# Kernel optimization log

Measured on AMD Instinct MI355X. Metric: run time of the kernel, lower is better.

## Reference

```python
import jax, jax.numpy as jnp
import numpy as np

B, S, H, NH = 2, 2048, 1024, 16
HD = H // NH
EPS = 1e-6

def rotate_half(x):
    x1, x2 = jnp.split(x, 2, axis=-1)
    return jnp.concatenate([-x2, x1], axis=-1)

def setup_inputs() -> dict:
    key = jax.random.key(0)
    ks = jax.random.split(key, 4)
    x = jax.random.normal(ks[0], (B, S, H), dtype=jnp.float32)
    # rotary angles
    inv_freq = 1.0 / (10000.0 ** (np.arange(0, HD, 2, dtype=np.float32) / HD))
    t = np.arange(S, dtype=np.float32)
    freqs = np.einsum('s,d->sd', t, inv_freq)
    emb = np.concatenate([freqs, freqs], axis=-1)  # [S, HD]
    cos = jnp.broadcast_to(jnp.cos(emb)[None], (B, S, HD)).astype(jnp.float32)
    sin = jnp.broadcast_to(jnp.sin(emb)[None], (B, S, HD)).astype(jnp.float32)
    attn_mask = jnp.broadcast_to(jnp.tril(jnp.ones((S, S), jnp.float32))[None], (B, S, S))
    W_uvqk = jax.random.normal(ks[1], (4 * H, H), dtype=jnp.float32) * (1.0 / np.sqrt(H))
    b_uvqk = jnp.zeros((4 * H,), jnp.float32)
    gate_w = jnp.ones((H,), jnp.float32)
    W_out = jax.random.normal(ks[2], (H, H), dtype=jnp.float32) * (1.0 / np.sqrt(H))
    b_out = jnp.zeros((H,), jnp.float32)
    return {"x": x, "cos": cos, "sin": sin, "attn_mask": attn_mask,
            "W_uvqk": W_uvqk, "b_uvqk": b_uvqk, "gate_w": gate_w,
            "W_out": W_out, "b_out": b_out}

def reference(x, cos, sin, attn_mask, W_uvqk, b_uvqk, gate_w, W_out, b_out):
    b, s, h = x.shape
    residual = x
    uvqk = jnp.einsum('bsh,oh->bso', x, W_uvqk) + b_uvqk
    u, v, q, k = jnp.split(uvqk, 4, axis=-1)
    u = jax.nn.silu(u)
    q = q.reshape(b, s, NH, HD)
    k = k.reshape(b, s, NH, HD)
    v = v.reshape(b, s, NH, HD)
    c = cos[:, :, None, :]  # [B,S,1,HD] broadcasts over heads
    sn = sin[:, :, None, :]
    q = q * c + rotate_half(q) * sn
    k = k * c + rotate_half(k) * sn
    # [B,NH,S,S] raw scores -> silu (no softmax) -> mask -> AV
    scores = jnp.einsum('bqnd,bknd->bnqk', q, k) / np.sqrt(HD).astype(np.float32)
    attn = jax.nn.silu(scores) * attn_mask[:, None, :, :]
    attn_out = jnp.einsum('bnqk,bknd->bqnd', attn, v).reshape(b, s, h)
    # RMSNorm (fp32) gating
    ao32 = attn_out.astype(jnp.float32)
    var = jnp.mean(ao32 * ao32, axis=-1, keepdims=True)
    normed = (gate_w * (ao32 * jax.lax.rsqrt(var + EPS))).astype(x.dtype)
    gated = normed * u
    out = jnp.einsum('bsh,oh->bso', gated, W_out) + b_out
    return residual + out
```

## Files before the change

kernel.cpp:

```cpp
#include <hip/hip_runtime.h>

typedef __attribute__((ext_vector_type(4))) float f32x4;
typedef __attribute__((ext_vector_type(8))) short short8;

static __device__ __forceinline__ unsigned short f2bf(float f) {
    union { float f; unsigned int u; } v; v.f = f;
    unsigned int r = v.u + 0x7FFFu + ((v.u >> 16) & 1u);
    return (unsigned short)(r >> 16);
}

static __device__ __forceinline__ float bf2f(unsigned short h) {
    union { unsigned int u; float f; } v; v.u = ((unsigned int)h) << 16;
    return v.f;
}

static __device__ __forceinline__ unsigned int cvt_pk_bf16(float lo, float hi) {
    unsigned int r;
    asm("v_cvt_pk_bf16_f32 %0, %1, %2" : "=v"(r) : "v"(lo), "v"(hi));
    return r;
}

static __device__ __forceinline__ void gload16(const void* g, void* l) {
    __builtin_amdgcn_global_load_lds(
        (const __attribute__((address_space(1))) unsigned int*)g,
        (__attribute__((address_space(3))) unsigned int*)l, 16, 0, 0);
}

static __device__ __forceinline__ void block_sync_raw() {
    asm volatile("" ::: "memory");
    __builtin_amdgcn_s_barrier();
    asm volatile("" ::: "memory");
}

__global__ __launch_bounds__(256) void k_convert(
    const float* __restrict__ x, const float* __restrict__ wu, const float* __restrict__ wo,
    unsigned short* __restrict__ xb, unsigned short* __restrict__ wub, unsigned short* __restrict__ wob)
{
    int i = blockIdx.x * 256 + threadIdx.x;
    const float* src; unsigned short* dst; int off;
    if (i < 1048576)       { src = x;  dst = xb;  off = i; }
    else if (i < 2097152)  { src = wu; dst = wub; off = i - 1048576; }
    else                   { src = wo; dst = wob; off = i - 2097152; }
    float4 v = reinterpret_cast<const float4*>(src)[off];
    ushort4 o;
    o.x = f2bf(v.x); o.y = f2bf(v.y); o.z = f2bf(v.z); o.w = f2bf(v.w);
    reinterpret_cast<ushort4*>(dst)[off] = o;
}

__global__ __launch_bounds__(256) void k_gemm0(
    const unsigned short* __restrict__ A, const unsigned short* __restrict__ Bmat,
    const float* __restrict__ bias,
    unsigned short* __restrict__ u_out, unsigned short* __restrict__ q_out,
    unsigned short* __restrict__ k_out, unsigned short* __restrict__ vt_out,
    const float* __restrict__ cosp, const float* __restrict__ sinp)
{
    const int K = 1024;
    constexpr int NT = 16;
    constexpr int ASZ = 64 * 64;
    constexpr int BSZ = 128 * 64;
    __shared__ __align__(16) unsigned short S[2 * (ASZ + BSZ)];
    int tid = threadIdx.x;
    int lane = tid & 63, wid = tid >> 6;
    int lo = lane & 15, q4 = lane >> 4;
    int x7 = lo & 7;
    int wr = wid >> 1, wc = wid & 1;
    int bm = blockIdx.x, bn = blockIdx.y;
    const unsigned short* Abase = A + (size_t)bm * 64 * K;
    const unsigned short* Bbase = Bmat + (size_t)bn * 128 * K;

    auto stage = [&](int bb, int kt) {
        unsigned short* As = S + bb * (ASZ + BSZ);
        unsigned short* Bs = As + ASZ;
#pragma unroll
        for (int j = 0; j < 2; ++j) {
            int ch = tid + j * 256;
            int r = ch >> 3, p = ch & 7;
            gload16(Abase + (size_t)r * K + kt * 64 + (p ^ (r & 7)) * 8, As + ch * 8);
        }
#pragma unroll
        for (int j = 0; j < 4; ++j) {
            int ch = tid + j * 256;
            int r = ch >> 3, p = ch & 7;
            gload16(Bbase + (size_t)r * K + kt * 64 + (p ^ (r & 7)) * 8, Bs + ch * 8);
        }
    };

    f32x4 acc[2][4] = {};
    stage(0, 0);
    int buf = 0;
    for (int kt = 0; kt < NT; ++kt) {
        if (kt + 1 < NT) {
            stage(buf ^ 1, kt + 1);
            asm volatile("s_waitcnt vmcnt(6)" ::: "memory");
        } else {
            asm volatile("s_waitcnt vmcnt(0)" ::: "memory");
        }
        block_sync_raw();
        const unsigned short* As = S + buf * (ASZ + BSZ);
        const unsigned short* Bs = As + ASZ;
#pragma unroll
        for (int kc = 0; kc < 2; ++kc) {
            int cRd = (kc * 4 + q4) ^ x7;
            short8 af[2], bfr[4];
#pragma unroll
            for (int t = 0; t < 2; ++t)
                af[t] = *(const short8*)&As[(wr * 32 + t * 16 + lo) * 64 + cRd * 8];
#pragma unroll
            for (int t = 0; t < 4; ++t)
                bfr[t] = *(const short8*)&Bs[(wc * 64 + t * 16 + lo) * 64 + cRd * 8];
#pragma unroll
            for (int mt = 0; mt < 2; ++mt)
#pragma unroll
                for (int nt = 0; nt < 4; ++nt)
                    acc[mt][nt] = __builtin_amdgcn_mfma_f32_16x16x32_bf16(af[mt], bfr[nt], acc[mt][nt], 0, 0, 0);
        }
        block_sync_raw();
        buf ^= 1;
    }

    int rowb = bm * 64 + wr * 32;
    int colb = bn * 128 + wc * 64;
    int region = bn >> 3;
    if (region == 1) {
        unsigned short* T = S;
#pragma unroll
        for (int mt = 0; mt < 2; ++mt)
#pragma unroll
            for (int nt = 0; nt < 4; ++nt) {
                float bcol = bias[colb + nt * 16 + lo];
                uint2 w;
                w.x = cvt_pk_bf16(acc[mt][nt][0] + bcol, acc[mt][nt][1] + bcol);
                w.y = cvt_pk_bf16(acc[mt][nt][2] + bcol, acc[mt][nt][3] + bcol);
                int c_local = wc * 64 + nt * 16 + lo;
                int schunk = wr * 4 + mt * 2 + (q4 >> 1);
                *(uint2*)((char*)T + c_local * 128 + ((schunk ^ (c_local & 7)) * 16) + (q4 & 1) * 8) = w;
            }
        __syncthreads();
        int c_row = tid >> 1;
        int bchunk = (tid & 1) * 4;
        int c_global = (bn - 8) * 128 + c_row;
        int head = c_global >> 6, d = c_global & 63;
        int batch = bm >> 5;
        int s_base = (bm * 64) & 2047;
        unsigned short* vrow = vt_out + ((size_t)(batch * 16 + head) * 64 + d) * 2048;
#pragma unroll
        for (int i = 0; i < 4; ++i) {
            int chunk = bchunk + i;
            uint4 v = *(const uint4*)((const char*)T + c_row * 128 + ((chunk ^ (c_row & 7)) * 16));
            *(uint4*)&vrow[s_base + chunk * 8] = v;
        }
    } else {
#pragma unroll
        for (int mt = 0; mt < 2; ++mt) {
#pragma unroll
            for (int r = 0; r < 4; ++r) {
                int rg = rowb + mt * 16 + q4 * 4 + r;
                int b = rg >> 11, s = rg & 2047;
                float vals[4];
#pragma unroll
                for (int nt = 0; nt < 4; ++nt)
                    vals[nt] = acc[mt][nt][r] + bias[colb + nt * 16 + lo];
                if (region == 0) {
#pragma unroll
                    for (int nt = 0; nt < 4; ++nt) {
                        float vv = vals[nt];
                        u_out[(size_t)rg * 1024 + colb + nt * 16 + lo] = f2bf(vv / (1.f + __expf(-vv)));
                    }
                } else {
                    const float* cb = cosp + (size_t)(b * 2048 + s) * 64;
                    const float* sb = sinp + (size_t)(b * 2048 + s) * 64;
                    float o[4];
#pragma unroll
                    for (int nt = 0; nt < 4; ++nt) {
                        int hd = nt * 16 + lo;
                        float partner = (nt < 2) ? -vals[nt + 2] : vals[nt - 2];
                        o[nt] = vals[nt] * cb[hd] + partner * sb[hd];
                    }
                    int c0 = colb - ((region == 2) ? 2048 : 3072);
                    unsigned short* dst = (region == 2) ? q_out : k_out;
#pragma unroll
                    for (int nt = 0; nt < 4; ++nt) {
                        int c = c0 + nt * 16 + lo;
                        int head = c >> 6, d = c & 63;
                        dst[((size_t)(b * 16 + head) * 2048 + s) * 64 + d] = f2bf(o[nt]);
                    }
                }
            }
        }
    }
}

__global__ __launch_bounds__(256) void k_gemm1(
    const unsigned short* __restrict__ A, const unsigned short* __restrict__ Bmat,
    const float* __restrict__ bias, const float* __restrict__ resid, float* __restrict__ out)
{
    const int K = 1024;
    constexpr int NT = 16;
    constexpr int ASZ = 64 * 64;
    constexpr int BSZ = 128 * 64;
    __shared__ __align__(16) unsigned short S[2 * (ASZ + BSZ)];
    int tid = threadIdx.x;
    int lane = tid & 63, wid = tid >> 6;
    int lo = lane & 15, q4 = lane >> 4;
    int x7 = lo & 7;
    int wr = wid >> 1, wc = wid & 1;
    int bn = blockIdx.x, bm = blockIdx.y;
    const unsigned short* Abase = A + (size_t)bm * 64 * K;
    const unsigned short* Bbase = Bmat + (size_t)bn * 128 * K;

    auto stage = [&](int bb, int kt) {
        unsigned short* As = S + bb * (ASZ + BSZ);
        unsigned short* Bs = As + ASZ;
#pragma unroll
        for (int j = 0; j < 2; ++j) {
            int ch = tid + j * 256;
            int r = ch >> 3, p = ch & 7;
            gload16(Abase + (size_t)r * K + kt * 64 + (p ^ (r & 7)) * 8, As + ch * 8);
        }
#pragma unroll
        for (int j = 0; j < 4; ++j) {
            int ch = tid + j * 256;
            int r = ch >> 3, p = ch & 7;
            gload16(Bbase + (size_t)r * K + kt * 64 + (p ^ (r & 7)) * 8, Bs + ch * 8);
        }
    };

    f32x4 acc[2][4] = {};
    stage(0, 0);
    int buf = 0;
    for (int kt = 0; kt < NT; ++kt) {
        if (kt + 1 < NT) {
            stage(buf ^ 1, kt + 1);
            asm volatile("s_waitcnt vmcnt(6)" ::: "memory");
        } else {
            asm volatile("s_waitcnt vmcnt(0)" ::: "memory");
        }
        block_sync_raw();
        const unsigned short* As = S + buf * (ASZ + BSZ);
        const unsigned short* Bs = As + ASZ;
#pragma unroll
        for (int kc = 0; kc < 2; ++kc) {
            int cRd = (kc * 4 + q4) ^ x7;
            short8 af[2], bfr[4];
#pragma unroll
            for (int t = 0; t < 2; ++t)
                af[t] = *(const short8*)&As[(wr * 32 + t * 16 + lo) * 64 + cRd * 8];
#pragma unroll
            for (int t = 0; t < 4; ++t)
                bfr[t] = *(const short8*)&Bs[(wc * 64 + t * 16 + lo) * 64 + cRd * 8];
#pragma unroll
            for (int mt = 0; mt < 2; ++mt)
#pragma unroll
                for (int nt = 0; nt < 4; ++nt)
                    acc[mt][nt] = __builtin_amdgcn_mfma_f32_16x16x32_bf16(af[mt], bfr[nt], acc[mt][nt], 0, 0, 0);
        }
        block_sync_raw();
        buf ^= 1;
    }

    int rowb = bm * 64 + wr * 32;
    int colb = bn * 128 + wc * 64;
#pragma unroll
    for (int mt = 0; mt < 2; ++mt)
#pragma unroll
        for (int r = 0; r < 4; ++r) {
            int rg = rowb + mt * 16 + q4 * 4 + r;
#pragma unroll
            for (int nt = 0; nt < 4; ++nt) {
                int c = colb + nt * 16 + lo;
                out[(size_t)rg * 1024 + c] = acc[mt][nt][r] + bias[c] + resid[(size_t)rg * 1024 + c];
            }
        }
}

__global__ __launch_bounds__(256) void k_attn(
    const unsigned short* __restrict__ Q, const unsigned short* __restrict__ Kg,
    const unsigned short* __restrict__ Vt_g, unsigned short* __restrict__ AO0,
    unsigned short* __restrict__ AO1)
{
    __shared__ __align__(16) unsigned short Ksb[2][64 * 64];
    __shared__ __align__(16) unsigned short Vsb[2][64 * 64];
    __shared__ __align__(16) unsigned short Ps[4 * 2048];
    int tid = threadIdx.x;
    int lane = tid & 63, wid = tid >> 6;
    int lo = lane & 15, q4 = lane >> 4;
    int bid = blockIdx.x;
    int bh = bid & 31;
    int s  = bid >> 5;
    int b = bh >> 4, head = bh & 15;

    const unsigned short* Qb = Q    + (size_t)bh * 2048 * 64;
    const unsigned short* Kb = Kg   + (size_t)bh * 2048 * 64;
    const unsigned short* Vb = Vt_g + (size_t)bh * 64 * 2048;
    unsigned short* Pw = Ps + wid * 2048;

    int i0 = wid * 128 + lane;
    int i1 = wid * 128 + 64 + lane;
    int c_0 = i0 & 7, r_0 = i0 >> 3;
    int c_1 = i1 & 7, r_1 = i1 >> 3;
    int cs0 = c_0 ^ (r_0 & 7), cs1 = c_1 ^ (r_1 & 7);
    size_t kOff0 = (size_t)r_0 * 64 + cs0 * 8,  kOff1 = (size_t)r_1 * 64 + cs1 * 8;
    size_t vOff0 = (size_t)r_0 * 2048 + cs0 * 8, vOff1 = (size_t)r_1 * 2048 + cs1 * 8;

    int x7 = lo & 7, qr_rel = q4 >> 1;
    char* pw0 = (char*)Pw + (lo)      * 128 + (q4 & 1) * 8;
    char* pw1 = (char*)Pw + (lo + 16) * 128 + (q4 & 1) * 8;
    int swz[8];
#pragma unroll
    for (int cc = 0; cc < 8; ++cc) swz[cc] = (cc ^ x7) * 16;
    const short8* prd[2][2];
#pragma unroll
    for (int kc = 0; kc < 2; ++kc) {
        prd[0][kc] = (const short8*)&Pw[(lo) * 64      + (((kc * 4 + q4) ^ x7) * 8)];
        prd[1][kc] = (const short8*)&Pw[(16 + lo) * 64 + (((kc * 4 + q4) ^ x7) * 8)];
    }

    auto stage = [&](int bb, int kt) {
        gload16(Kb + (size_t)kt * 4096 + kOff0, &Ksb[bb][i0 * 8]);
        gload16(Kb + (size_t)kt * 4096 + kOff1, &Ksb[bb][i1 * 8]);
        gload16(Vb + (size_t)kt * 64 + vOff0, &Vsb[bb][i0 * 8]);
        gload16(Vb + (size_t)kt * 64 + vOff1, &Vsb[bb][i1 * 8]);
    };

    int J = s;
    int q0w = J * 128 + wid * 32;
    short8 qf[2][2];
#pragma unroll
    for (int qt = 0; qt < 2; ++qt)
#pragma unroll
        for (int kc = 0; kc < 2; ++kc)
            qf[qt][kc] = *(const short8*)(Qb + (size_t)(q0w + qt * 16 + lo) * 64 + kc * 32 + q4 * 8);

    f32x4 oacc[2][4] = {};
    stage(0, 0);
    __syncthreads();
    int buf = 0;

    for (int t = 0; t < 17; ++t) {
        int kt = (t <= s) ? t : (t + 15 - 2 * s);
        if (t < 16) {
            int tn = t + 1;
            int ktn = (tn <= s) ? tn : (tn + 15 - 2 * s);
            stage(buf ^ 1, ktn);
        }
        if (64 * kt <= q0w + 31) {
            f32x4 sacc[4][2] = {};
#pragma unroll
            for (int kc = 0; kc < 2; ++kc)
#pragma unroll
                for (int kt4 = 0; kt4 < 4; ++kt4) {
                    short8 kf = *(const short8*)&Ksb[buf][(kt4 * 16 + lo) * 64 + (((kc * 4 + q4) ^ x7) * 8)];
#pragma unroll
                    for (int qt = 0; qt < 2; ++qt)
                        sacc[kt4][qt] = __builtin_amdgcn_mfma_f32_16x16x32_bf16(kf, qf[qt][kc], sacc[kt4][qt], 0, 0, 0);
                }
            bool needMask = (64 * kt + 63 > q0w);
#pragma unroll
            for (int kt4 = 0; kt4 < 4; ++kt4)
#pragma unroll
                for (int qt = 0; qt < 2; ++qt) {
                    int qc = qt * 16 + lo;
                    float p[4];
#pragma unroll
                    for (int rr = 0; rr < 4; ++rr) {
                        float S = sacc[kt4][qt][rr];
                        float e = __builtin_amdgcn_exp2f(S * -0.180336880f);
                        float pv = S * 0.125f * __builtin_amdgcn_rcpf(1.f + e);
                        if (needMask) {
                            int ky = kt * 64 + kt4 * 16 + q4 * 4 + rr;
                            if (ky > q0w + qc) pv = 0.f;
                        }
                        p[rr] = pv;
                    }
                    uint2 w;
                    w.x = cvt_pk_bf16(p[0], p[1]);
                    w.y = cvt_pk_bf16(p[2], p[3]);
                    *(uint2*)(((qt == 0) ? pw0 : pw1) + swz[kt4 * 2 + qr_rel]) = w;
                }
#pragma unroll
            for (int kc = 0; kc < 2; ++kc) {
                short8 pf0 = *prd[0][kc];
                short8 pf1 = *prd[1][kc];
#pragma unroll
                for (int nt = 0; nt < 4; ++nt) {
                    short8 vf = *(const short8*)&Vsb[buf][(nt * 16 + lo) * 64 + (((kc * 4 + q4) ^ x7) * 8)];
                    oacc[0][nt] = __builtin_amdgcn_mfma_f32_16x16x32_bf16(pf0, vf, oacc[0][nt], 0, 0, 0);
                    oacc[1][nt] = __builtin_amdgcn_mfma_f32_16x16x32_bf16(pf1, vf, oacc[1][nt], 0, 0, 0);
                }
            }
        }
        if (t == s) {
            unsigned short* aoLane = AO0 + ((size_t)(b * 2048 + q0w + q4 * 4)) * 1024 + head * 64 + lo;
#pragma unroll
            for (int qt = 0; qt < 2; ++qt)
#pragma unroll
                for (int nt = 0; nt < 4; ++nt)
#pragma unroll
                    for (int rr = 0; rr < 4; ++rr) {
                        aoLane[(qt * 16 + rr) * 1024 + nt * 16] = f2bf(oacc[qt][nt][rr]);
                        oacc[qt][nt][rr] = 0.f;
                    }
            J = 15 - s;
            q0w = J * 128 + wid * 32;
#pragma unroll
            for (int qt = 0; qt < 2; ++qt)
#pragma unroll
                for (int kc = 0; kc < 2; ++kc)
                    qf[qt][kc] = *(const short8*)(Qb + (size_t)(q0w + qt * 16 + lo) * 64 + kc * 32 + q4 * 8);
        }
        __syncthreads();
        buf ^= 1;
    }
    unsigned short* aoLane = AO1 + ((size_t)(b * 2048 + q0w + q4 * 4)) * 1024 + head * 64 + lo;
#pragma unroll
    for (int qt = 0; qt < 2; ++qt)
#pragma unroll
        for (int nt = 0; nt < 4; ++nt)
#pragma unroll
            for (int rr = 0; rr < 4; ++rr)
                aoLane[(qt * 16 + rr) * 1024 + nt * 16] = f2bf(oacc[qt][nt][rr]);
}

__global__ __launch_bounds__(256) void k_rmsgate(
    const unsigned short* __restrict__ AO0, const unsigned short* __restrict__ AO1,
    const unsigned short* __restrict__ U,
    const float* __restrict__ gw, unsigned short* __restrict__ G)
{
    __shared__ float red[4];
    int row = blockIdx.x, t = threadIdx.x;
    ushort4 a0v = *(const ushort4*)&AO0[(size_t)row * 1024 + t * 4];
    ushort4 a1v = *(const ushort4*)&AO1[(size_t)row * 1024 + t * 4];
    float4 a;
    a.x = bf2f(a0v.x) + bf2f(a1v.x);
    a.y = bf2f(a0v.y) + bf2f(a1v.y);
    a.z = bf2f(a0v.z) + bf2f(a1v.z);
    a.w = bf2f(a0v.w) + bf2f(a1v.w);
    float ss = a.x * a.x + a.y * a.y + a.z * a.z + a.w * a.w;
#pragma unroll
    for (int off = 32; off; off >>= 1) ss += __shfl_down(ss, off);
    int wid = t >> 6, lane = t & 63;
    if (lane == 0) red[wid] = ss;
    __syncthreads();
    float tot = red[0] + red[1] + red[2] + red[3];
    float rs = rsqrtf(tot * (1.f / 1024.f) + 1e-6f);
    float4 g = *(const float4*)&gw[t * 4];
    ushort4 uv = *(const ushort4*)&U[(size_t)row * 1024 + t * 4];
    ushort4 o;
    o.x = f2bf(g.x * a.x * rs * bf2f(uv.x));
    o.y = f2bf(g.y * a.y * rs * bf2f(uv.y));
    o.z = f2bf(g.z * a.z * rs * bf2f(uv.z));
    o.w = f2bf(g.w * a.w * rs * bf2f(uv.w));
    *(ushort4*)&G[(size_t)row * 1024 + t * 4] = o;
}

extern "C" void kernel_launch(void* const* d_in, const int* in_sizes, int n_in,
                              void* d_out, int out_size, void* d_ws, size_t ws_size,
                              hipStream_t stream) {
    const float* x      = (const float*)d_in[0];
    const float* cosp   = (const float*)d_in[1];
    const float* sinp   = (const float*)d_in[2];
    const float* b_uvqk = (const float*)d_in[5];
    const float* gate_w = (const float*)d_in[6];
    const float* b_out  = (const float*)d_in[8];
    float* out = (float*)d_out;

    char* ws = (char*)d_ws;
    unsigned short* xb  = (unsigned short*)(ws);
    unsigned short* wub = (unsigned short*)(ws + 8388608);
    unsigned short* wob = (unsigned short*)(ws + 16777216);
    unsigned short* ub  = (unsigned short*)(ws + 18874368);
    unsigned short* qb  = (unsigned short*)(ws + 35651584);
    unsigned short* kb  = (unsigned short*)(ws + 44040192);
    unsigned short* vtb = (unsigned short*)(ws + 52428800);
    unsigned short* aob = (unsigned short*)(ws + 60817408);
    unsigned short* gb  = (unsigned short*)(ws + 77594624);
    unsigned short* ao1 = (unsigned short*)(ws);

    k_convert<<<9216, 256, 0, stream>>>((const float*)d_in[0], (const float*)d_in[4],
                                        (const float*)d_in[7], xb, wub, wob);
    k_gemm0<<<dim3(64, 32), 256, 0, stream>>>(xb, wub, b_uvqk, ub, qb, kb, vtb, cosp, sinp);
    k_attn<<<512, 256, 0, stream>>>(qb, kb, vtb, aob, ao1);
    k_rmsgate<<<4096, 256, 0, stream>>>(aob, ao1, ub, gate_w, gb);
    k_gemm1<<<dim3(8, 64), 256, 0, stream>>>(gb, wob, b_out, x, out);
}
```

Measured before the change: 120.9 us.

## Split attention KV loop across two blocks per tile with partial-sum buffers

Each attention block's 17-step key loop is split into two halves run by separate blocks (1024 blocks instead of 512). Each half writes its bf16 partial outputs, or zeros, into its own buffer pair, and the RMS-gate kernel sums four partials instead of two. This aims to fill more CUs on the MI355X and cut per-block latency. The cost is extra global writes and reads for the partials, extra rounding from storing partials in bf16, and reuse of the xb/wub workspace as scratch.

```diff
diff --git a/kernel.cpp b/kernel.cpp
--- a/kernel.cpp
+++ b/kernel.cpp
@@ -275,8 +275,9 @@
 
 __global__ __launch_bounds__(256) void k_attn(
     const unsigned short* __restrict__ Q, const unsigned short* __restrict__ Kg,
-    const unsigned short* __restrict__ Vt_g, unsigned short* __restrict__ AO0,
-    unsigned short* __restrict__ AO1)
+    const unsigned short* __restrict__ Vt_g,
+    unsigned short* __restrict__ P1a, unsigned short* __restrict__ P1b,
+    unsigned short* __restrict__ P2a, unsigned short* __restrict__ P2b)
 {
     __shared__ __align__(16) unsigned short Ksb[2][64 * 64];
     __shared__ __align__(16) unsigned short Vsb[2][64 * 64];
@@ -286,8 +287,12 @@
     int lo = lane & 15, q4 = lane >> 4;
     int bid = blockIdx.x;
     int bh = bid & 31;
-    int s  = bid >> 5;
+    int s  = (bid >> 5) & 15;
+    int h  = bid >> 9;
     int b = bh >> 4, head = bh & 15;
+    unsigned short* P1 = h ? P1b : P1a;
+    unsigned short* P2 = h ? P2b : P2a;
+    int t0 = h ? 9 : 0, t1 = h ? 17 : 9;
 
     const unsigned short* Qb = Q    + (size_t)bh * 2048 * 64;
     const unsigned short* Kb = Kg   + (size_t)bh * 2048 * 64;
@@ -321,8 +326,31 @@
         gload16(Vb + (size_t)kt * 64 + vOff0, &Vsb[bb][i0 * 8]);
         gload16(Vb + (size_t)kt * 64 + vOff1, &Vsb[bb][i1 * 8]);
     };
-
-    int J = s;
+    auto ktof = [&](int u) { return (u <= s) ? u : (u + 15 - 2 * s); };
+
+    f32x4 oacc[2][4] = {};
+    auto storeP = [&](unsigned short* bufp, int q0x) {
+        unsigned short* p = bufp + ((size_t)(b * 2048 + q0x + q4 * 4)) * 1024 + head * 64 + lo;
+#pragma unroll
+        for (int qt = 0; qt < 2; ++qt)
+#pragma unroll
+            for (int nt = 0; nt < 4; ++nt)
+#pragma unroll
+                for (int rr = 0; rr < 4; ++rr)
+                    p[(qt * 16 + rr) * 1024 + nt * 16] = f2bf(oacc[qt][nt][rr]);
+    };
+    auto zeroP = [&](unsigned short* bufp, int q0x) {
+        unsigned short* p = bufp + ((size_t)(b * 2048 + q0x + q4 * 4)) * 1024 + head * 64 + lo;
+#pragma unroll
+        for (int qt = 0; qt < 2; ++qt)
+#pragma unroll
+            for (int nt = 0; nt < 4; ++nt)
+#pragma unroll
+                for (int rr = 0; rr < 4; ++rr)
+                    p[(qt * 16 + rr) * 1024 + nt * 16] = 0;
+    };
+
+    int J = (t0 <= s) ? s : 15 - s;
     int q0w = J * 128 + wid * 32;
     short8 qf[2][2];
 #pragma unroll
@@ -331,18 +359,14 @@
         for (int kc = 0; kc < 2; ++kc)
             qf[qt][kc] = *(const short8*)(Qb + (size_t)(q0w + qt * 16 + lo) * 64 + kc * 32 + q4 * 8);
 
-    f32x4 oacc[2][4] = {};
-    stage(0, 0);
+    stage(0, ktof(t0));
     __syncthreads();
     int buf = 0;
-
-    for (int t = 0; t < 17; ++t) {
-        int kt = (t <= s) ? t : (t + 15 - 2 * s);
-        if (t < 16) {
-            int tn = t + 1;
-            int ktn = (tn <= s) ? tn : (tn + 15 - 2 * s);
-            stage(buf ^ 1, ktn);
-        }
+    bool stored1 = false;
+
+    for (int t = t0; t < t1; ++t) {
+        if (t + 1 < t1) stage(buf ^ 1, ktof(t + 1));
+        int kt = ktof(t);
         if (64 * kt <= q0w + 31) {
             f32x4 sacc[4][2] = {};
 #pragma unroll
@@ -390,16 +414,14 @@
             }
         }
         if (t == s) {
-            unsigned short* aoLane = AO0 + ((size_t)(b * 2048 + q0w + q4 * 4)) * 1024 + head * 64 + lo;
+            storeP(P1, q0w);
 #pragma unroll
             for (int qt = 0; qt < 2; ++qt)
 #pragma unroll
                 for (int nt = 0; nt < 4; ++nt)
 #pragma unroll
-                    for (int rr = 0; rr < 4; ++rr) {
-                        aoLane[(qt * 16 + rr) * 1024 + nt * 16] = f2bf(oacc[qt][nt][rr]);
-                        oacc[qt][nt][rr] = 0.f;
-                    }
+                    for (int rr = 0; rr < 4; ++rr) oacc[qt][nt][rr] = 0.f;
+            stored1 = true;
             J = 15 - s;
             q0w = J * 128 + wid * 32;
 #pragma unroll
@@ -411,30 +433,33 @@
         __syncthreads();
         buf ^= 1;
     }
-    unsigned short* aoLane = AO1 + ((size_t)(b * 2048 + q0w + q4 * 4)) * 1024 + head * 64 + lo;
-#pragma unroll
-    for (int qt = 0; qt < 2; ++qt)
-#pragma unroll
-        for (int nt = 0; nt < 4; ++nt)
-#pragma unroll
-            for (int rr = 0; rr < 4; ++rr)
-                aoLane[(qt * 16 + rr) * 1024 + nt * 16] = f2bf(oacc[qt][nt][rr]);
+
+    if (!stored1 && J == s) {
+        storeP(P1, s * 128 + wid * 32);
+        zeroP(P2, (15 - s) * 128 + wid * 32);
+    } else {
+        storeP(P2, (15 - s) * 128 + wid * 32);
+        if (!stored1) zeroP(P1, s * 128 + wid * 32);
+    }
 }
 
 __global__ __launch_bounds__(256) void k_rmsgate(
-    const unsigned short* __restrict__ AO0, const unsigned short* __restrict__ AO1,
+    const unsigned short* __restrict__ P1a, const unsigned short* __restrict__ P1b,
+    const unsigned short* __restrict__ P2a, const unsigned short* __restrict__ P2b,
     const unsigned short* __restrict__ U,
     const float* __restrict__ gw, unsigned short* __restrict__ G)
 {
     __shared__ float red[4];
     int row = blockIdx.x, t = threadIdx.x;
-    ushort4 a0v = *(const ushort4*)&AO0[(size_t)row * 1024 + t * 4];
-    ushort4 a1v = *(const ushort4*)&AO1[(size_t)row * 1024 + t * 4];
+    ushort4 v0 = *(const ushort4*)&P1a[(size_t)row * 1024 + t * 4];
+    ushort4 v1 = *(const ushort4*)&P1b[(size_t)row * 1024 + t * 4];
+    ushort4 v2 = *(const ushort4*)&P2a[(size_t)row * 1024 + t * 4];
+    ushort4 v3 = *(const ushort4*)&P2b[(size_t)row * 1024 + t * 4];
     float4 a;
-    a.x = bf2f(a0v.x) + bf2f(a1v.x);
-    a.y = bf2f(a0v.y) + bf2f(a1v.y);
-    a.z = bf2f(a0v.z) + bf2f(a1v.z);
-    a.w = bf2f(a0v.w) + bf2f(a1v.w);
+    a.x = bf2f(v0.x) + bf2f(v1.x) + bf2f(v2.x) + bf2f(v3.x);
+    a.y = bf2f(v0.y) + bf2f(v1.y) + bf2f(v2.y) + bf2f(v3.y);
+    a.z = bf2f(v0.z) + bf2f(v1.z) + bf2f(v2.z) + bf2f(v3.z);
+    a.w = bf2f(v0.w) + bf2f(v1.w) + bf2f(v2.w) + bf2f(v3.w);
     float ss = a.x * a.x + a.y * a.y + a.z * a.z + a.w * a.w;
 #pragma unroll
     for (int off = 32; off; off >>= 1) ss += __shfl_down(ss, off);
@@ -472,14 +497,16 @@
     unsigned short* qb  = (unsigned short*)(ws + 35651584);
     unsigned short* kb  = (unsigned short*)(ws + 44040192);
     unsigned short* vtb = (unsigned short*)(ws + 52428800);
-    unsigned short* aob = (unsigned short*)(ws + 60817408);
+    unsigned short* p1a = (unsigned short*)(ws + 60817408);
+    unsigned short* p1b = (unsigned short*)(ws + 69206016);
     unsigned short* gb  = (unsigned short*)(ws + 77594624);
-    unsigned short* ao1 = (unsigned short*)(ws);
+    unsigned short* p2a = xb;
+    unsigned short* p2b = wub;
 
     k_convert<<<9216, 256, 0, stream>>>((const float*)d_in[0], (const float*)d_in[4],
                                         (const float*)d_in[7], xb, wub, wob);
     k_gemm0<<<dim3(64, 32), 256, 0, stream>>>(xb, wub, b_uvqk, ub, qb, kb, vtb, cosp, sinp);
-    k_attn<<<512, 256, 0, stream>>>(qb, kb, vtb, aob, ao1);
-    k_rmsgate<<<4096, 256, 0, stream>>>(aob, ao1, ub, gate_w, gb);
+    k_attn<<<1024, 256, 0, stream>>>(qb, kb, vtb, p1a, p1b, p2a, p2b);
+    k_rmsgate<<<4096, 256, 0, stream>>>(p1a, p1b, p2a, p2b, ub, gate_w, gb);
     k_gemm1<<<dim3(8, 64), 256, 0, stream>>>(gb, wob, b_out, x, out);
 }
```

New measurement: 125.6 us (median of 2 runs). 1.04x slower.
